# Optimization experiments

Hardware: AMD Instinct MI355X
Metric: run time of the kernel (lower is better)

The kernel has to match this reference:

```python
import jax, jax.numpy as jnp
import numpy as np

THRESH = 0.5
MARGIN = 0.1
SCALE_POS = 2.0
SCALE_NEG = 40.0
EPSILON = 1e-5


def setup_inputs() -> dict:
    key = jax.random.key(0)
    k1, k2, k3 = jax.random.split(key, 3)
    B, D = 8192, 1024
    feats = jax.random.normal(k1, (B, D), dtype=jnp.float32)
    labels = jax.random.randint(k2, (B,), 0, 128, dtype=jnp.int64)
    score = jax.random.normal(k3, (B, 3), dtype=jnp.float32)
    return {"feats": feats, "labels": labels, "score": score, "type_idx": 1}


def reference(feats, labels, score, type_idx):
    B = feats.shape[0]
    # L2 normalize (torch F.normalize eps=1e-12)
    norm = jnp.maximum(jnp.linalg.norm(feats, axis=1, keepdims=True), 1e-12)
    f = feats / norm
    sim = f @ f.T  # [B, B]

    tmp = jnp.argmax(score, axis=-1) == type_idx          # [B] selected samples
    eq = labels[:, None] == labels[None, :]               # same-label
    pair = tmp[:, None] & tmp[None, :]                    # both selected

    mask_pos_all = pair & eq                              # includes diagonal, like torch mask[i]
    count = jnp.sum(mask_pos_all, axis=1)                 # torch: sum(mask[i])
    pos0 = mask_pos_all & (sim < 1.0 - EPSILON)           # pos_pair_ after <1-eps filter
    neg0 = pair & (~eq)                                   # neg_pair_

    min_pos = jnp.min(jnp.where(pos0, sim, jnp.inf), axis=1)   # min(pos_pair_)
    max_neg = jnp.max(jnp.where(neg0, sim, -jnp.inf), axis=1)  # max(neg_pair_)

    neg_sel = neg0 & (sim + MARGIN > min_pos[:, None])    # hard negatives
    pos_sel = pos0 & (sim - MARGIN < max_neg[:, None])    # hard positives

    valid = (tmp & (count > 1)
             & jnp.any(pos0, axis=1) & jnp.any(neg0, axis=1)
             & jnp.any(neg_sel, axis=1) & jnp.any(pos_sel, axis=1))

    pos_sum = jnp.sum(jnp.where(pos_sel, jnp.exp(-SCALE_POS * (sim - THRESH)), 0.0), axis=1)
    neg_sum = jnp.sum(jnp.where(neg_sel, jnp.exp(SCALE_NEG * (sim - THRESH)), 0.0), axis=1)
    row_loss = jnp.log1p(pos_sum) / SCALE_POS + jnp.log1p(neg_sum) / SCALE_NEG

    return jnp.sum(jnp.where(valid, row_loss, 0.0)) / B
```

## Files before the change

### kernel.cpp

```cpp
#include <hip/hip_runtime.h>
#include <hip/hip_bf16.h>

typedef __attribute__((ext_vector_type(8))) short bf16x8;
typedef __attribute__((ext_vector_type(4))) float f32x4;


#define OFF_META    0
#define OFF_IDXSEL  (64*1024)
#define OFF_LBLSEL  (96*1024)
#define OFF_RLOSS   (160*1024)
#define OFF_FSEL    (256*1024)

__device__ inline unsigned short f2bf(float f){
    union { __hip_bfloat16 h; unsigned short u; } cv;
    cv.h = __float2bfloat16(f);
    return cv.u;
}

__global__ __launch_bounds__(256) void select_kernel(
    const float* __restrict__ score, const int* __restrict__ type_idx,
    const void* __restrict__ labels_raw,
    int* __restrict__ idx_sel, int* __restrict__ labels_sel,
    int* meta, int B)
{
    int tid = threadIdx.x, lane = tid & 63, wid = tid >> 6;
    int row = blockIdx.x * 256 + tid;
    __shared__ int s_is64, s_wcnt[4], s_base;

    if (wid == 0) {
        int hi = ((const int*)labels_raw)[2 * lane + 1];
        unsigned long long nz = __ballot(hi != 0);
        if (lane == 0) s_is64 = (nz == 0ULL) ? 1 : 0;
    }

    int f = 0;
    if (row < B) {
        float s0 = score[3*row], s1 = score[3*row+1], s2 = score[3*row+2];
        int am = 0; float b = s0;
        if (s1 > b) { b = s1; am = 1; }
        if (s2 > b) { am = 2; }
        f = (am == type_idx[0]) ? 1 : 0;
    }
    unsigned long long m = __ballot(f != 0);
    int incl = __popcll(m & ((2ULL << lane) - 1ULL));
    if (lane == 0) s_wcnt[wid] = __popcll(m);
    __syncthreads();
    if (tid == 0)
        s_base = atomicAdd(&meta[0], s_wcnt[0] + s_wcnt[1] + s_wcnt[2] + s_wcnt[3]);
    __syncthreads();
    if (f) {
        int prefix = 0;
        for (int w = 0; w < wid; w++) prefix += s_wcnt[w];
        int pos = s_base + prefix + incl - 1;
        idx_sel[pos] = row;
        labels_sel[pos] = s_is64 ? (int)((const long long*)labels_raw)[row]
                                 : ((const int*)labels_raw)[row];
    }
}

__global__ __launch_bounds__(256) void gather_kernel(
    const float* __restrict__ feats, const int* __restrict__ idx_sel,
    const int* __restrict__ meta, unsigned short* __restrict__ fsel, int D)
{
    int S = meta[0];
    int Spad = (S + 127) & ~127;
    int s = blockIdx.x * 4 + (threadIdx.x >> 6);
    if (s >= Spad) return;
    int lane = threadIdx.x & 63;
    ushort4* dst = (ushort4*)(fsel + (size_t)s * D);

    if (s >= S) {
        ushort4 z = {0,0,0,0};
        for (int i = lane; i < (D >> 2); i += 64) dst[i] = z;
        return;
    }

    int r = idx_sel[s];
    const float4* src = (const float4*)(feats + (size_t)r * D);

    if (D == 1024) {
        float4 v[4];
#pragma unroll
        for (int i = 0; i < 4; i++) v[i] = src[lane + i * 64];
        float ssq = 0.f;
#pragma unroll
        for (int i = 0; i < 4; i++)
            ssq += v[i].x*v[i].x + v[i].y*v[i].y + v[i].z*v[i].z + v[i].w*v[i].w;
        for (int o = 32; o; o >>= 1) ssq += __shfl_down(ssq, o);
        ssq = __shfl(ssq, 0);
        float sc = 1.0f / fmaxf(sqrtf(ssq), 1e-12f);
#pragma unroll
        for (int i = 0; i < 4; i++) {
            ushort4 o;
            o.x = f2bf(v[i].x * sc); o.y = f2bf(v[i].y * sc);
            o.z = f2bf(v[i].z * sc); o.w = f2bf(v[i].w * sc);
            dst[lane + i * 64] = o;
        }
    } else {
        int nv = D >> 2;
        float ssq = 0.f;
        for (int i = lane; i < nv; i += 64) {
            float4 v = src[i];
            ssq += v.x*v.x + v.y*v.y + v.z*v.z + v.w*v.w;
        }
        for (int o = 32; o; o >>= 1) ssq += __shfl_down(ssq, o);
        ssq = __shfl(ssq, 0);
        float sc = 1.0f / fmaxf(sqrtf(ssq), 1e-12f);
        for (int i = lane; i < nv; i += 64) {
            float4 v = src[i];
            ushort4 o;
            o.x = f2bf(v.x * sc); o.y = f2bf(v.y * sc);
            o.z = f2bf(v.z * sc); o.w = f2bf(v.w * sc);
            dst[i] = o;
        }
    }
}

__global__ __launch_bounds__(512) void simgemm_kernel(
    const unsigned short* __restrict__ fsel, const int* __restrict__ meta,
    float* __restrict__ sim, int D)
{
    int S = meta[0];
    int Spad = (S + 127) & ~127;
    int bm = blockIdx.x * 128, bn = blockIdx.y * 128;
    if (bm >= Spad || bn >= Spad) return;
    if (bm > bn) return;

    __shared__ unsigned short lA[2][1024 * 8];
    __shared__ unsigned short lB[2][1024 * 8];

    int tid = threadIdx.x;
    int lane = tid & 63;
    int wave = tid >> 6;
    int wr = (wave >> 2) * 64;
    int wc = (wave & 3) * 32;
    int laneRow = lane & 15;
    int laneK = lane >> 4;

    f32x4 acc[4][2];
#pragma unroll
    for (int m = 0; m < 4; m++)
#pragma unroll
        for (int n = 0; n < 2; n++)
            acc[m][n] = (f32x4){0.f, 0.f, 0.f, 0.f};

#define STAGE(buf, k0)                                                        \
    _Pragma("unroll")                                                         \
    for (int p = 0; p < 2; p++) {                                             \
        int c = tid + p * 512;                                                \
        int r = c >> 3, slot = c & 7;                                         \
        int og = slot ^ (r & 7);                                              \
        __builtin_amdgcn_global_load_lds(                                     \
            (const __attribute__((address_space(1))) unsigned int*)           \
                (fsel + (size_t)(bm + r) * D + (k0) + og * 8),                \
            (__attribute__((address_space(3))) unsigned int*)&lA[buf][c * 8], \
            16, 0, 0);                                                        \
        __builtin_amdgcn_global_load_lds(                                     \
            (const __attribute__((address_space(1))) unsigned int*)           \
                (fsel + (size_t)(bn + r) * D + (k0) + og * 8),                \
            (__attribute__((address_space(3))) unsigned int*)&lB[buf][c * 8], \
            16, 0, 0);                                                        \
    }

    int nt = D >> 6;
    STAGE(0, 0)
    int cur = 0;
    for (int t = 0; t < nt; t++) {
        if (t + 1 < nt) {
            STAGE(cur ^ 1, (t + 1) << 6)
            asm volatile("s_waitcnt vmcnt(4)" ::: "memory");
        } else {
            asm volatile("s_waitcnt vmcnt(0)" ::: "memory");
        }
        __builtin_amdgcn_s_barrier();
        __builtin_amdgcn_sched_barrier(0);

        bf16x8 af[2][4], bfr[2][2];
#pragma unroll
        for (int s2 = 0; s2 < 2; s2++) {
            int o = s2 * 4 + laneK;
#pragma unroll
            for (int m = 0; m < 4; m++) {
                int row = wr + m * 16 + laneRow;
                af[s2][m] = *(const bf16x8*)&lA[cur][(row * 8 + (o ^ (row & 7))) * 8];
            }
#pragma unroll
            for (int n = 0; n < 2; n++) {
                int row = wc + n * 16 + laneRow;
                bfr[s2][n] = *(const bf16x8*)&lB[cur][(row * 8 + (o ^ (row & 7))) * 8];
            }
        }
#pragma unroll
        for (int s2 = 0; s2 < 2; s2++)
#pragma unroll
            for (int m = 0; m < 4; m++)
#pragma unroll
                for (int n = 0; n < 2; n++)
                    acc[m][n] = __builtin_amdgcn_mfma_f32_16x16x32_bf16(
                        af[s2][m], bfr[s2][n], acc[m][n], 0, 0, 0);

        __builtin_amdgcn_sched_barrier(0);
        __builtin_amdgcn_s_barrier();
        cur ^= 1;
    }
#undef STAGE

#pragma unroll
    for (int m = 0; m < 4; m++) {
        int row0 = bm + wr + m * 16 + (lane >> 4) * 4;
#pragma unroll
        for (int n = 0; n < 2; n++) {
            int col = bn + wc + n * 16 + laneRow;
#pragma unroll
            for (int q = 0; q < 4; q++)
                sim[(size_t)(row0 + q) * Spad + col] = acc[m][n][q];
            if (bm != bn) {
                *(f32x4*)&sim[(size_t)col * Spad + row0] = acc[m][n];
            }
        }
    }
}

__global__ __launch_bounds__(256) void loss_kernel(
    const float* __restrict__ sim, const int* __restrict__ labels_sel,
    const int* __restrict__ meta, float* __restrict__ row_loss)
{
    int S = meta[0];
    if (blockIdx.x * 4 >= S) return;
    int Spad = (S + 127) & ~127;
    int tid = threadIdx.x;
    __shared__ unsigned char slbl[8192];
    for (int j = tid; j < Spad; j += 256)
        slbl[j] = (j < S) ? (unsigned char)labels_sel[j] : 0xFF;
    __syncthreads();

    int lane = tid & 63;
    int s = blockIdx.x * 4 + (tid >> 6);
    if (s >= S) return;

    const float4* rowv = (const float4*)(sim + (size_t)s * Spad);
    const unsigned* lblv = (const unsigned*)slbl;
    const float ONE_ME = 1.0f - 1e-5f;
    int lbl = slbl[s];
    int nv = Spad >> 2;
    float rl = 0.f;

    if (nv <= 704) {
        float4 rv[11];
        unsigned lw[11];
#pragma unroll
        for (int i = 0; i < 11; i++) {
            int j4 = lane + i * 64;
            if (j4 < nv) { rv[i] = rowv[j4]; lw[i] = lblv[j4]; }
            else         { rv[i] = (float4){0,0,0,0}; lw[i] = 0xFFFFFFFFu; }
        }
        int cnt = 0;
        float minp = INFINITY, maxn = -INFINITY;
#pragma unroll
        for (int i = 0; i < 11; i++) {
            int j0 = (lane + i * 64) << 2;
#pragma unroll
            for (int e = 0; e < 4; e++) {
                float sv = (&rv[i].x)[e];
                if (j0 + e == s) sv = 1.0f;
                int lb = (lw[i] >> (8 * e)) & 0xFF;
                if (lb == lbl) {
                    cnt++;
                    if (sv < ONE_ME) minp = fminf(minp, sv);
                } else if (lb != 0xFF) {
                    maxn = fmaxf(maxn, sv);
                }
            }
        }
        for (int o = 32; o; o >>= 1) {
            cnt += __shfl_down(cnt, o);
            minp = fminf(minp, __shfl_down(minp, o));
            maxn = fmaxf(maxn, __shfl_down(maxn, o));
        }
        cnt  = __shfl(cnt, 0);
        minp = __shfl(minp, 0);
        maxn = __shfl(maxn, 0);

        if (cnt > 1 && minp < 3e38f && maxn > -3e38f) {
            float psum = 0.f, nsum = 0.f;
#pragma unroll
            for (int i = 0; i < 11; i++) {
                int j0 = (lane + i * 64) << 2;
#pragma unroll
                for (int e = 0; e < 4; e++) {
                    float sv = (&rv[i].x)[e];
                    if (j0 + e == s) sv = 1.0f;
                    int lb = (lw[i] >> (8 * e)) & 0xFF;
                    if (lb == lbl) {
                        if (sv < ONE_ME && sv - 0.1f < maxn)
                            psum += __expf(-2.0f * (sv - 0.5f));
                    } else if (lb != 0xFF) {
                        if (sv + 0.1f > minp)
                            nsum += __expf(40.0f * (sv - 0.5f));
                    }
                }
            }
            for (int o = 32; o; o >>= 1) {
                psum += __shfl_down(psum, o);
                nsum += __shfl_down(nsum, o);
            }
            if (psum > 0.f && nsum > 0.f)
                rl = log1pf(psum) * 0.5f + log1pf(nsum) * 0.025f;
        }
    } else {
        int cnt = 0;
        float minp = INFINITY, maxn = -INFINITY;
        for (int j4 = lane; j4 < nv; j4 += 64) {
            float4 v = rowv[j4];
            unsigned w = lblv[j4];
#pragma unroll
            for (int e = 0; e < 4; e++) {
                int j = (j4 << 2) + e;
                float sv = (&v.x)[e];
                if (j == s) sv = 1.0f;
                int lb = (w >> (8 * e)) & 0xFF;
                if (lb == lbl) {
                    cnt++;
                    if (sv < ONE_ME) minp = fminf(minp, sv);
                } else if (lb != 0xFF) {
                    maxn = fmaxf(maxn, sv);
                }
            }
        }
        for (int o = 32; o; o >>= 1) {
            cnt += __shfl_down(cnt, o);
            minp = fminf(minp, __shfl_down(minp, o));
            maxn = fmaxf(maxn, __shfl_down(maxn, o));
        }
        cnt  = __shfl(cnt, 0);
        minp = __shfl(minp, 0);
        maxn = __shfl(maxn, 0);

        if (cnt > 1 && minp < 3e38f && maxn > -3e38f) {
            float psum = 0.f, nsum = 0.f;
            for (int j4 = lane; j4 < nv; j4 += 64) {
                float4 v = rowv[j4];
                unsigned w = lblv[j4];
#pragma unroll
                for (int e = 0; e < 4; e++) {
                    int j = (j4 << 2) + e;
                    float sv = (&v.x)[e];
                    if (j == s) sv = 1.0f;
                    int lb = (w >> (8 * e)) & 0xFF;
                    if (lb == lbl) {
                        if (sv < ONE_ME && sv - 0.1f < maxn)
                            psum += __expf(-2.0f * (sv - 0.5f));
                    } else if (lb != 0xFF) {
                        if (sv + 0.1f > minp)
                            nsum += __expf(40.0f * (sv - 0.5f));
                    }
                }
            }
            for (int o = 32; o; o >>= 1) {
                psum += __shfl_down(psum, o);
                nsum += __shfl_down(nsum, o);
            }
            if (psum > 0.f && nsum > 0.f)
                rl = log1pf(psum) * 0.5f + log1pf(nsum) * 0.025f;
        }
    }
    if (lane == 0) row_loss[s] = rl;
}

__global__ __launch_bounds__(256) void reduce_kernel(
    const float* __restrict__ row_loss, const int* __restrict__ meta,
    float* out, float invB)
{
    int S = meta[0];
    float sum = 0.f;
    for (int j = threadIdx.x; j < S; j += 256) sum += row_loss[j];
    for (int o = 32; o; o >>= 1) sum += __shfl_down(sum, o);
    __shared__ float sm[4];
    if ((threadIdx.x & 63) == 0) sm[threadIdx.x >> 6] = sum;
    __syncthreads();
    if (threadIdx.x == 0) out[0] = (sm[0] + sm[1] + sm[2] + sm[3]) * invB;
}

extern "C" void kernel_launch(void* const* d_in, const int* in_sizes, int n_in,
                              void* d_out, int out_size, void* d_ws, size_t ws_size,
                              hipStream_t stream)
{
    const float* feats    = (const float*)d_in[0];
    const void*  labels   = d_in[1];
    const float* score    = (const float*)d_in[2];
    const int*   type_idx = (const int*)d_in[3];

    int B = in_sizes[1];
    int D = in_sizes[0] / B;

    char* ws = (char*)d_ws;
    int*   meta       = (int*)  (ws + OFF_META);
    int*   idx_sel    = (int*)  (ws + OFF_IDXSEL);
    int*   labels_sel = (int*)  (ws + OFF_LBLSEL);
    float* row_loss   = (float*)(ws + OFF_RLOSS);
    unsigned short* fsel = (unsigned short*)(ws + OFF_FSEL);
    float* sim        = (float*)(ws + OFF_FSEL + (size_t)B * D * 2);
    float* out        = (float*)d_out;

    (void)hipMemsetAsync(meta, 0, 16, stream);

    select_kernel<<<(B + 255) / 256, 256, 0, stream>>>(score, type_idx, labels,
                                                       idx_sel, labels_sel, meta, B);
    gather_kernel<<<B / 4, 256, 0, stream>>>(feats, idx_sel, meta, fsel, D);
    dim3 g(B / 128, B / 128);
    simgemm_kernel<<<g, 512, 0, stream>>>(fsel, meta, sim, D);
    loss_kernel<<<B / 4, 256, 0, stream>>>(sim, labels_sel, meta, row_loss);
    reduce_kernel<<<1, 256, 0, stream>>>(row_loss, meta, out, 1.0f / (float)B);
}
```

Baseline: 140.4 us.

## Persistent triangular GEMM with triple-buffered LDS and fused final reduction

The similarity GEMM now launches 256 persistent blocks instead of a full B/128 x B/128 grid. Each block walks upper-triangular tile indices, decoding the tile coordinates with a sqrt formula plus correction loops. This removes the many blocks that exit immediately. The K loop moves from double to triple buffering in one shared array, so two loads are in flight per step, at the cost of more LDS per block. The separate reduce kernel is folded into the loss kernel using an atomic last-block counter on meta[3], which saves one launch but relies on meta being zeroed by the existing memset.

```diff
diff --git a/kernel.cpp b/kernel.cpp
--- a/kernel.cpp
+++ b/kernel.cpp
@@ -122,12 +122,10 @@
 {
     int S = meta[0];
     int Spad = (S + 127) & ~127;
-    int bm = blockIdx.x * 128, bn = blockIdx.y * 128;
-    if (bm >= Spad || bn >= Spad) return;
-    if (bm > bn) return;
-
-    __shared__ unsigned short lA[2][1024 * 8];
-    __shared__ unsigned short lB[2][1024 * 8];
+    int T = Spad >> 7;
+    int total = T * (T + 1) / 2;
+
+    __shared__ unsigned short smem[49152];
 
     int tid = threadIdx.x;
     int lane = tid & 63;
@@ -136,249 +134,268 @@
     int wc = (wave & 3) * 32;
     int laneRow = lane & 15;
     int laneK = lane >> 4;
-
-    f32x4 acc[4][2];
-#pragma unroll
-    for (int m = 0; m < 4; m++)
-#pragma unroll
-        for (int n = 0; n < 2; n++)
-            acc[m][n] = (f32x4){0.f, 0.f, 0.f, 0.f};
-
-#define STAGE(buf, k0)                                                        \
+    int nt = D >> 6;
+
+#define STAGE(buf, k0, bm_, bn_)                                              \
     _Pragma("unroll")                                                         \
     for (int p = 0; p < 2; p++) {                                             \
         int c = tid + p * 512;                                                \
         int r = c >> 3, slot = c & 7;                                         \
         int og = slot ^ (r & 7);                                              \
+        int bb = (buf) * 16384;                                               \
         __builtin_amdgcn_global_load_lds(                                     \
             (const __attribute__((address_space(1))) unsigned int*)           \
-                (fsel + (size_t)(bm + r) * D + (k0) + og * 8),                \
-            (__attribute__((address_space(3))) unsigned int*)&lA[buf][c * 8], \
+                (fsel + (size_t)((bm_) + r) * D + (k0) + og * 8),             \
+            (__attribute__((address_space(3))) unsigned int*)&smem[bb + c * 8],\
             16, 0, 0);                                                        \
         __builtin_amdgcn_global_load_lds(                                     \
             (const __attribute__((address_space(1))) unsigned int*)           \
-                (fsel + (size_t)(bn + r) * D + (k0) + og * 8),                \
-            (__attribute__((address_space(3))) unsigned int*)&lB[buf][c * 8], \
+                (fsel + (size_t)((bn_) + r) * D + (k0) + og * 8),             \
+            (__attribute__((address_space(3))) unsigned int*)                 \
+                &smem[bb + 8192 + c * 8],                                     \
             16, 0, 0);                                                        \
     }
 
-    int nt = D >> 6;
-    STAGE(0, 0)
-    int cur = 0;
-    for (int t = 0; t < nt; t++) {
-        if (t + 1 < nt) {
-            STAGE(cur ^ 1, (t + 1) << 6)
-            asm volatile("s_waitcnt vmcnt(4)" ::: "memory");
-        } else {
-            asm volatile("s_waitcnt vmcnt(0)" ::: "memory");
-        }
-        __builtin_amdgcn_s_barrier();
-        __builtin_amdgcn_sched_barrier(0);
-
-        bf16x8 af[2][4], bfr[2][2];
-#pragma unroll
-        for (int s2 = 0; s2 < 2; s2++) {
-            int o = s2 * 4 + laneK;
-#pragma unroll
-            for (int m = 0; m < 4; m++) {
-                int row = wr + m * 16 + laneRow;
-                af[s2][m] = *(const bf16x8*)&lA[cur][(row * 8 + (o ^ (row & 7))) * 8];
+    for (int t = blockIdx.x; t < total; t += gridDim.x) {
+        float bq = 2.0f * T + 1.0f;
+        int ti = (int)((bq - sqrtf(bq * bq - 8.0f * (float)t)) * 0.5f);
+        if (ti >= T) ti = T - 1;
+        while (ti > 0 && (ti * T - ti * (ti - 1) / 2) > t) ti--;
+        while (((ti + 1) * T - (ti + 1) * ti / 2) <= t) ti++;
+        int tj = ti + (t - (ti * T - ti * (ti - 1) / 2));
+        int bm = ti << 7, bn = tj << 7;
+
+        f32x4 acc[4][2];
+#pragma unroll
+        for (int m = 0; m < 4; m++)
+#pragma unroll
+            for (int n = 0; n < 2; n++)
+                acc[m][n] = (f32x4){0.f, 0.f, 0.f, 0.f};
+
+        STAGE(0, 0, bm, bn)
+        if (nt > 1) STAGE(1, 64, bm, bn)
+
+        for (int k = 0; k < nt; k++) {
+            if (k + 2 < nt) STAGE((k + 2) % 3, (k + 2) << 6, bm, bn)
+            int rem = nt - 1 - k;
+            if (rem >= 2)      asm volatile("s_waitcnt vmcnt(8)" ::: "memory");
+            else if (rem == 1) asm volatile("s_waitcnt vmcnt(4)" ::: "memory");
+            else               asm volatile("s_waitcnt vmcnt(0)" ::: "memory");
+            __builtin_amdgcn_s_barrier();
+            __builtin_amdgcn_sched_barrier(0);
+
+            int bb = (k % 3) * 16384;
+            bf16x8 af[2][4], bfr[2][2];
+#pragma unroll
+            for (int s2 = 0; s2 < 2; s2++) {
+                int o = s2 * 4 + laneK;
+#pragma unroll
+                for (int m = 0; m < 4; m++) {
+                    int row = wr + m * 16 + laneRow;
+                    af[s2][m] = *(const bf16x8*)&smem[bb + (row * 8 + (o ^ (row & 7))) * 8];
+                }
+#pragma unroll
+                for (int n = 0; n < 2; n++) {
+                    int row = wc + n * 16 + laneRow;
+                    bfr[s2][n] = *(const bf16x8*)&smem[bb + 8192 + (row * 8 + (o ^ (row & 7))) * 8];
+                }
             }
 #pragma unroll
+            for (int s2 = 0; s2 < 2; s2++)
+#pragma unroll
+                for (int m = 0; m < 4; m++)
+#pragma unroll
+                    for (int n = 0; n < 2; n++)
+                        acc[m][n] = __builtin_amdgcn_mfma_f32_16x16x32_bf16(
+                            af[s2][m], bfr[s2][n], acc[m][n], 0, 0, 0);
+
+            __builtin_amdgcn_sched_barrier(0);
+            __builtin_amdgcn_s_barrier();
+        }
+
+#pragma unroll
+        for (int m = 0; m < 4; m++) {
+            int row0 = bm + wr + m * 16 + (lane >> 4) * 4;
+#pragma unroll
             for (int n = 0; n < 2; n++) {
-                int row = wc + n * 16 + laneRow;
-                bfr[s2][n] = *(const bf16x8*)&lB[cur][(row * 8 + (o ^ (row & 7))) * 8];
+                int col = bn + wc + n * 16 + laneRow;
+#pragma unroll
+                for (int q = 0; q < 4; q++)
+                    sim[(size_t)(row0 + q) * Spad + col] = acc[m][n][q];
+                if (bm != bn) {
+                    *(f32x4*)&sim[(size_t)col * Spad + row0] = acc[m][n];
+                }
             }
         }
-#pragma unroll
-        for (int s2 = 0; s2 < 2; s2++)
-#pragma unroll
-            for (int m = 0; m < 4; m++)
-#pragma unroll
-                for (int n = 0; n < 2; n++)
-                    acc[m][n] = __builtin_amdgcn_mfma_f32_16x16x32_bf16(
-                        af[s2][m], bfr[s2][n], acc[m][n], 0, 0, 0);
-
-        __builtin_amdgcn_sched_barrier(0);
-        __builtin_amdgcn_s_barrier();
-        cur ^= 1;
     }
 #undef STAGE
-
-#pragma unroll
-    for (int m = 0; m < 4; m++) {
-        int row0 = bm + wr + m * 16 + (lane >> 4) * 4;
-#pragma unroll
-        for (int n = 0; n < 2; n++) {
-            int col = bn + wc + n * 16 + laneRow;
-#pragma unroll
-            for (int q = 0; q < 4; q++)
-                sim[(size_t)(row0 + q) * Spad + col] = acc[m][n][q];
-            if (bm != bn) {
-                *(f32x4*)&sim[(size_t)col * Spad + row0] = acc[m][n];
-            }
-        }
-    }
 }
 
 __global__ __launch_bounds__(256) void loss_kernel(
     const float* __restrict__ sim, const int* __restrict__ labels_sel,
-    const int* __restrict__ meta, float* __restrict__ row_loss)
+    int* __restrict__ meta, float* __restrict__ row_loss,
+    float* out, float invB)
 {
     int S = meta[0];
-    if (blockIdx.x * 4 >= S) return;
     int Spad = (S + 127) & ~127;
     int tid = threadIdx.x;
     __shared__ unsigned char slbl[8192];
-    for (int j = tid; j < Spad; j += 256)
-        slbl[j] = (j < S) ? (unsigned char)labels_sel[j] : 0xFF;
+    __shared__ float sm[4];
+    __shared__ int isLast;
+
+    bool blockActive = ((int)blockIdx.x * 4 < S);
+    if (blockActive) {
+        for (int j = tid; j < Spad; j += 256)
+            slbl[j] = (j < S) ? (unsigned char)labels_sel[j] : 0xFF;
+        __syncthreads();
+
+        int lane = tid & 63;
+        int s = blockIdx.x * 4 + (tid >> 6);
+        if (s < S) {
+            const float4* rowv = (const float4*)(sim + (size_t)s * Spad);
+            const unsigned* lblv = (const unsigned*)slbl;
+            const float ONE_ME = 1.0f - 1e-5f;
+            int lbl = slbl[s];
+            int nv = Spad >> 2;
+            float rl = 0.f;
+
+            if (nv <= 704) {
+                float4 rv[11];
+                unsigned lw[11];
+#pragma unroll
+                for (int i = 0; i < 11; i++) {
+                    int j4 = lane + i * 64;
+                    if (j4 < nv) { rv[i] = rowv[j4]; lw[i] = lblv[j4]; }
+                    else         { rv[i] = (float4){0,0,0,0}; lw[i] = 0xFFFFFFFFu; }
+                }
+                int cnt = 0;
+                float minp = INFINITY, maxn = -INFINITY;
+#pragma unroll
+                for (int i = 0; i < 11; i++) {
+                    int j0 = (lane + i * 64) << 2;
+#pragma unroll
+                    for (int e = 0; e < 4; e++) {
+                        float sv = (&rv[i].x)[e];
+                        if (j0 + e == s) sv = 1.0f;
+                        int lb = (lw[i] >> (8 * e)) & 0xFF;
+                        if (lb == lbl) {
+                            cnt++;
+                            if (sv < ONE_ME) minp = fminf(minp, sv);
+                        } else if (lb != 0xFF) {
+                            maxn = fmaxf(maxn, sv);
+                        }
+                    }
+                }
+                for (int o = 32; o; o >>= 1) {
+                    cnt += __shfl_down(cnt, o);
+                    minp = fminf(minp, __shfl_down(minp, o));
+                    maxn = fmaxf(maxn, __shfl_down(maxn, o));
+                }
+                cnt  = __shfl(cnt, 0);
+                minp = __shfl(minp, 0);
+                maxn = __shfl(maxn, 0);
+
+                if (cnt > 1 && minp < 3e38f && maxn > -3e38f) {
+                    float psum = 0.f, nsum = 0.f;
+#pragma unroll
+                    for (int i = 0; i < 11; i++) {
+                        int j0 = (lane + i * 64) << 2;
+#pragma unroll
+                        for (int e = 0; e < 4; e++) {
+                            float sv = (&rv[i].x)[e];
+                            if (j0 + e == s) sv = 1.0f;
+                            int lb = (lw[i] >> (8 * e)) & 0xFF;
+                            if (lb == lbl) {
+                                if (sv < ONE_ME && sv - 0.1f < maxn)
+                                    psum += __expf(-2.0f * (sv - 0.5f));
+                            } else if (lb != 0xFF) {
+                                if (sv + 0.1f > minp)
+                                    nsum += __expf(40.0f * (sv - 0.5f));
+                            }
+                        }
+                    }
+                    for (int o = 32; o; o >>= 1) {
+                        psum += __shfl_down(psum, o);
+                        nsum += __shfl_down(nsum, o);
+                    }
+                    if (psum > 0.f && nsum > 0.f)
+                        rl = log1pf(psum) * 0.5f + log1pf(nsum) * 0.025f;
+                }
+            } else {
+                int cnt = 0;
+                float minp = INFINITY, maxn = -INFINITY;
+                for (int j4 = lane; j4 < nv; j4 += 64) {
+                    float4 v = rowv[j4];
+                    unsigned w = lblv[j4];
+#pragma unroll
+                    for (int e = 0; e < 4; e++) {
+                        int j = (j4 << 2) + e;
+                        float sv = (&v.x)[e];
+                        if (j == s) sv = 1.0f;
+                        int lb = (w >> (8 * e)) & 0xFF;
+                        if (lb == lbl) {
+                            cnt++;
+                            if (sv < ONE_ME) minp = fminf(minp, sv);
+                        } else if (lb != 0xFF) {
+                            maxn = fmaxf(maxn, sv);
+                        }
+                    }
+                }
+                for (int o = 32; o; o >>= 1) {
+                    cnt += __shfl_down(cnt, o);
+                    minp = fminf(minp, __shfl_down(minp, o));
+                    maxn = fmaxf(maxn, __shfl_down(maxn, o));
+                }
+                cnt  = __shfl(cnt, 0);
+                minp = __shfl(minp, 0);
+                maxn = __shfl(maxn, 0);
+
+                if (cnt > 1 && minp < 3e38f && maxn > -3e38f) {
+                    float psum = 0.f, nsum = 0.f;
+                    for (int j4 = lane; j4 < nv; j4 += 64) {
+                        float4 v = rowv[j4];
+                        unsigned w = lblv[j4];
+#pragma unroll
+                        for (int e = 0; e < 4; e++) {
+                            int j = (j4 << 2) + e;
+                            float sv = (&v.x)[e];
+                            if (j == s) sv = 1.0f;
+                            int lb = (w >> (8 * e)) & 0xFF;
+                            if (lb == lbl) {
+                                if (sv < ONE_ME && sv - 0.1f < maxn)
+                                    psum += __expf(-2.0f * (sv - 0.5f));
+                            } else if (lb != 0xFF) {
+                                if (sv + 0.1f > minp)
+                                    nsum += __expf(40.0f * (sv - 0.5f));
+                            }
+                        }
+                    }
+                    for (int o = 32; o; o >>= 1) {
+                        psum += __shfl_down(psum, o);
+                        nsum += __shfl_down(nsum, o);
+                    }
+                    if (psum > 0.f && nsum > 0.f)
+                        rl = log1pf(psum) * 0.5f + log1pf(nsum) * 0.025f;
+                }
+            }
+            if (lane == 0) row_loss[s] = rl;
+        }
+    }
+
+    if (tid == 0) {
+        __threadfence();
+        int done = atomicAdd(&meta[3], 1);
+        isLast = (done == (int)gridDim.x - 1) ? 1 : 0;
+    }
     __syncthreads();
-
-    int lane = tid & 63;
-    int s = blockIdx.x * 4 + (tid >> 6);
-    if (s >= S) return;
-
-    const float4* rowv = (const float4*)(sim + (size_t)s * Spad);
-    const unsigned* lblv = (const unsigned*)slbl;
-    const float ONE_ME = 1.0f - 1e-5f;
-    int lbl = slbl[s];
-    int nv = Spad >> 2;
-    float rl = 0.f;
-
-    if (nv <= 704) {
-        float4 rv[11];
-        unsigned lw[11];
-#pragma unroll
-        for (int i = 0; i < 11; i++) {
-            int j4 = lane + i * 64;
-            if (j4 < nv) { rv[i] = rowv[j4]; lw[i] = lblv[j4]; }
-            else         { rv[i] = (float4){0,0,0,0}; lw[i] = 0xFFFFFFFFu; }
-        }
-        int cnt = 0;
-        float minp = INFINITY, maxn = -INFINITY;
-#pragma unroll
-        for (int i = 0; i < 11; i++) {
-            int j0 = (lane + i * 64) << 2;
-#pragma unroll
-            for (int e = 0; e < 4; e++) {
-                float sv = (&rv[i].x)[e];
-                if (j0 + e == s) sv = 1.0f;
-                int lb = (lw[i] >> (8 * e)) & 0xFF;
-                if (lb == lbl) {
-                    cnt++;
-                    if (sv < ONE_ME) minp = fminf(minp, sv);
-                } else if (lb != 0xFF) {
-                    maxn = fmaxf(maxn, sv);
-                }
-            }
-        }
-        for (int o = 32; o; o >>= 1) {
-            cnt += __shfl_down(cnt, o);
-            minp = fminf(minp, __shfl_down(minp, o));
-            maxn = fmaxf(maxn, __shfl_down(maxn, o));
-        }
-        cnt  = __shfl(cnt, 0);
-        minp = __shfl(minp, 0);
-        maxn = __shfl(maxn, 0);
-
-        if (cnt > 1 && minp < 3e38f && maxn > -3e38f) {
-            float psum = 0.f, nsum = 0.f;
-#pragma unroll
-            for (int i = 0; i < 11; i++) {
-                int j0 = (lane + i * 64) << 2;
-#pragma unroll
-                for (int e = 0; e < 4; e++) {
-                    float sv = (&rv[i].x)[e];
-                    if (j0 + e == s) sv = 1.0f;
-                    int lb = (lw[i] >> (8 * e)) & 0xFF;
-                    if (lb == lbl) {
-                        if (sv < ONE_ME && sv - 0.1f < maxn)
-                            psum += __expf(-2.0f * (sv - 0.5f));
-                    } else if (lb != 0xFF) {
-                        if (sv + 0.1f > minp)
-                            nsum += __expf(40.0f * (sv - 0.5f));
-                    }
-                }
-            }
-            for (int o = 32; o; o >>= 1) {
-                psum += __shfl_down(psum, o);
-                nsum += __shfl_down(nsum, o);
-            }
-            if (psum > 0.f && nsum > 0.f)
-                rl = log1pf(psum) * 0.5f + log1pf(nsum) * 0.025f;
-        }
-    } else {
-        int cnt = 0;
-        float minp = INFINITY, maxn = -INFINITY;
-        for (int j4 = lane; j4 < nv; j4 += 64) {
-            float4 v = rowv[j4];
-            unsigned w = lblv[j4];
-#pragma unroll
-            for (int e = 0; e < 4; e++) {
-                int j = (j4 << 2) + e;
-                float sv = (&v.x)[e];
-                if (j == s) sv = 1.0f;
-                int lb = (w >> (8 * e)) & 0xFF;
-                if (lb == lbl) {
-                    cnt++;
-                    if (sv < ONE_ME) minp = fminf(minp, sv);
-                } else if (lb != 0xFF) {
-                    maxn = fmaxf(maxn, sv);
-                }
-            }
-        }
-        for (int o = 32; o; o >>= 1) {
-            cnt += __shfl_down(cnt, o);
-            minp = fminf(minp, __shfl_down(minp, o));
-            maxn = fmaxf(maxn, __shfl_down(maxn, o));
-        }
-        cnt  = __shfl(cnt, 0);
-        minp = __shfl(minp, 0);
-        maxn = __shfl(maxn, 0);
-
-        if (cnt > 1 && minp < 3e38f && maxn > -3e38f) {
-            float psum = 0.f, nsum = 0.f;
-            for (int j4 = lane; j4 < nv; j4 += 64) {
-                float4 v = rowv[j4];
-                unsigned w = lblv[j4];
-#pragma unroll
-                for (int e = 0; e < 4; e++) {
-                    int j = (j4 << 2) + e;
-                    float sv = (&v.x)[e];
-                    if (j == s) sv = 1.0f;
-                    int lb = (w >> (8 * e)) & 0xFF;
-                    if (lb == lbl) {
-                        if (sv < ONE_ME && sv - 0.1f < maxn)
-                            psum += __expf(-2.0f * (sv - 0.5f));
-                    } else if (lb != 0xFF) {
-                        if (sv + 0.1f > minp)
-                            nsum += __expf(40.0f * (sv - 0.5f));
-                    }
-                }
-            }
-            for (int o = 32; o; o >>= 1) {
-                psum += __shfl_down(psum, o);
-                nsum += __shfl_down(nsum, o);
-            }
-            if (psum > 0.f && nsum > 0.f)
-                rl = log1pf(psum) * 0.5f + log1pf(nsum) * 0.025f;
-        }
-    }
-    if (lane == 0) row_loss[s] = rl;
-}
-
-__global__ __launch_bounds__(256) void reduce_kernel(
-    const float* __restrict__ row_loss, const int* __restrict__ meta,
-    float* out, float invB)
-{
-    int S = meta[0];
-    float sum = 0.f;
-    for (int j = threadIdx.x; j < S; j += 256) sum += row_loss[j];
-    for (int o = 32; o; o >>= 1) sum += __shfl_down(sum, o);
-    __shared__ float sm[4];
-    if ((threadIdx.x & 63) == 0) sm[threadIdx.x >> 6] = sum;
-    __syncthreads();
-    if (threadIdx.x == 0) out[0] = (sm[0] + sm[1] + sm[2] + sm[3]) * invB;
+    if (isLast) {
+        float sum = 0.f;
+        for (int j = tid; j < S; j += 256) sum += row_loss[j];
+        for (int o = 32; o; o >>= 1) sum += __shfl_down(sum, o);
+        if ((tid & 63) == 0) sm[tid >> 6] = sum;
+        __syncthreads();
+        if (tid == 0) out[0] = (sm[0] + sm[1] + sm[2] + sm[3]) * invB;
+    }
 }
 
 extern "C" void kernel_launch(void* const* d_in, const int* in_sizes, int n_in,
@@ -407,8 +424,7 @@
     select_kernel<<<(B + 255) / 256, 256, 0, stream>>>(score, type_idx, labels,
                                                        idx_sel, labels_sel, meta, B);
     gather_kernel<<<B / 4, 256, 0, stream>>>(feats, idx_sel, meta, fsel, D);
-    dim3 g(B / 128, B / 128);
-    simgemm_kernel<<<g, 512, 0, stream>>>(fsel, meta, sim, D);
-    loss_kernel<<<B / 4, 256, 0, stream>>>(sim, labels_sel, meta, row_loss);
-    reduce_kernel<<<1, 256, 0, stream>>>(row_loss, meta, out, 1.0f / (float)B);
-}
+    simgemm_kernel<<<256, 512, 0, stream>>>(fsel, meta, sim, D);
+    loss_kernel<<<B / 4, 256, 0, stream>>>(sim, labels_sel, meta, row_loss,
+                                           out, 1.0f / (float)B);
+}
```

Result: slower. 147.2 us (+4.8%).
